# Kernel tuning notes

Hardware: AMD Instinct MI355X
Metric: run time of the kernel (lower is better)

## Reference

```python
import jax, jax.numpy as jnp
import numpy as np

D, H1, O, E = 1024, 4096, 1024, 8
B = 8192


def setup_inputs() -> dict:
    key = jax.random.key(0)
    k1, k2, k3, k4 = jax.random.split(key, 4)
    # kaiming_uniform_ with nonlinearity='relu': bound = sqrt(6 / fan_in), fan_in = last dim
    b_w1 = float(np.sqrt(6.0 / D))
    b_w2 = float(np.sqrt(6.0 / H1))
    x = jax.random.normal(k1, (B, D), dtype=jnp.float32)
    eid = jax.random.randint(k2, (B,), 0, E, dtype=jnp.int32)
    W1 = jax.random.uniform(k3, (E, H1, D), dtype=jnp.float32, minval=-b_w1, maxval=b_w1)
    W2 = jax.random.uniform(k4, (E, O, H1), dtype=jnp.float32, minval=-b_w2, maxval=b_w2)
    b2 = jnp.zeros((E, O), dtype=jnp.float32)
    return {"x": x, "eid": eid, "W1": W1, "W2": W2, "b2": b2}


def reference(x, eid, W1, W2, b2):
    # Per-token expert MLP: y_i = gelu(x_i @ W1[eid_i].T) @ W2[eid_i].T + b2[eid_i]
    # Dense-dispatch formulation: loop over the (small, static) expert axis,
    # compute each expert MLP on all tokens, and select per-token via mask.
    # Math is identical to the sort/gather/scatter original.
    y = jnp.zeros((x.shape[0], W2.shape[1]), dtype=x.dtype)
    for e in range(W1.shape[0]):
        h = jax.nn.gelu(x @ W1[e].T, approximate=False)   # [B, H1]
        y_e = h @ W2[e].T + b2[e]                          # [B, O]
        mask = (eid == e)[:, None].astype(x.dtype)
        y = y + mask * y_e
    return y
```

## Files before the change

kernel.cpp:

```cpp
#include <hip/hip_runtime.h>
#include <hip/hip_bf16.h>
#include <math.h>

constexpr int kD  = 1024;
constexpr int kH1 = 4096;
constexpr int kO  = 1024;
constexpr int kE  = 8;
constexpr int kB  = 8192;

constexpr int BM   = 128;
constexpr int MAXT = kB / BM + kE;

typedef __attribute__((ext_vector_type(8))) short short8;
typedef __attribute__((ext_vector_type(4))) float f32x4;

__device__ __forceinline__ unsigned short f2bf(float f) {
  unsigned int u = __float_as_uint(f);
  u += 0x7fffu + ((u >> 16) & 1u);
  return (unsigned short)(u >> 16);
}

__device__ __forceinline__ float gelu_fast(float x) {
  float u = 0.7978845608028654f * (x + 0.044715f * x * x * x);
  float eu = __expf(2.0f * u);
  float th = 1.0f - 2.0f / (eu + 1.0f);
  return 0.5f * x * (1.0f + th);
}

__device__ __forceinline__ void cvt8(const float* __restrict__ src,
                                     unsigned short* __restrict__ dst) {
  const float4* s = (const float4*)src;
  float4 f0 = s[0], f1 = s[1];
  short8 v;
  v[0] = (short)f2bf(f0.x); v[1] = (short)f2bf(f0.y);
  v[2] = (short)f2bf(f0.z); v[3] = (short)f2bf(f0.w);
  v[4] = (short)f2bf(f1.x); v[5] = (short)f2bf(f1.y);
  v[6] = (short)f2bf(f1.z); v[7] = (short)f2bf(f1.w);
  *(short8*)dst = v;
}

__global__ __launch_bounds__(256) void setup_kernel(const int* __restrict__ eid,
                                                    int* __restrict__ perm,
                                                    int* __restrict__ tiles) {
  __shared__ int cnt[kE];
  __shared__ int off[kE];
  __shared__ int cur[kE];
  int t = threadIdx.x;
  if (t < kE) { cnt[t] = 0; cur[t] = 0; }
  __syncthreads();
  for (int i = t; i < kB; i += 256) atomicAdd(&cnt[eid[i]], 1);
  __syncthreads();
  if (t == 0) {
    int o = 0, nt = 0;
    for (int e = 0; e < kE; ++e) {
      off[e] = o;
      int c = cnt[e];
      for (int r = 0; r < c; r += BM) {
        tiles[nt * 4 + 0] = e;
        tiles[nt * 4 + 1] = o + r;
        tiles[nt * 4 + 2] = (c - r < BM) ? (c - r) : BM;
        tiles[nt * 4 + 3] = 0;
        ++nt;
      }
      o += c;
    }
    for (; nt < MAXT; ++nt) {
      tiles[nt * 4 + 0] = 0; tiles[nt * 4 + 1] = 0;
      tiles[nt * 4 + 2] = 0; tiles[nt * 4 + 3] = 0;
    }
  }
  __syncthreads();
  for (int i = t; i < kB; i += 256) {
    int e = eid[i];
    int p = off[e] + atomicAdd(&cur[e], 1);
    perm[p] = i;
  }
}

constexpr int kGB = kB * kD / 8 / 256;
constexpr int kCN = kE * kH1 * kD / 8;

__global__ __launch_bounds__(256) void prep_kernel(
    const float* __restrict__ x, const int* __restrict__ perm,
    unsigned short* __restrict__ xg,
    const float* __restrict__ W1, unsigned short* __restrict__ W1b) {
  const int b = blockIdx.x;
  if (b < kGB) {
    int idx = b * 256 + threadIdx.x;
    int pos = idx >> 7;
    int c   = (idx & 127) << 3;
    cvt8(x + (size_t)perm[pos] * kD + c, xg + (size_t)pos * kD + c);
  } else {
    const int cb = b - kGB;
    const int stride = 2048 * 256;
    for (int i = cb * 256 + threadIdx.x; i < kCN; i += stride)
      cvt8(W1 + (size_t)i * 8, W1b + (size_t)i * 8);
  }
}

__global__ __launch_bounds__(256) void convert_kernel(const float* __restrict__ src,
                                                      unsigned short* __restrict__ dst,
                                                      int n8) {
  int stride = gridDim.x * 256;
  for (int i = blockIdx.x * 256 + threadIdx.x; i < n8; i += stride)
    cvt8(src + (size_t)i * 8, dst + (size_t)i * 8);
}

template <int KTOT, int N, int NPAN, int MODE, int CONVW2>
__global__ __launch_bounds__(512, 2) void gemm32_kernel(
    const unsigned short* __restrict__ Amat,
    const unsigned short* __restrict__ Bmat,
    const float* __restrict__ bias,
    const int* __restrict__ tiles,
    const int* __restrict__ perm,
    unsigned short* __restrict__ out_bf,
    float* __restrict__ out_f,
    const float* __restrict__ csrc,
    unsigned short* __restrict__ cdst) {
  extern __shared__ char lds[];
  constexpr int NKt = KTOT / 32;
  constexpr int TOTAL = MAXT * NPAN;
  constexpr int cpx = TOTAL / 8;
  constexpr int nchN = (NPAN >= 4) ? NPAN / 4 : 1;

  const int bid = blockIdx.x;
  const int t = threadIdx.x;

  if constexpr (CONVW2 > 0) {
    if (bid >= TOTAL) {
      const int cb = bid - TOTAL;
      constexpr int per = kCN / 512;
      size_t u0 = (size_t)cb * per;
      for (int i = t; i < per; i += 512)
        cvt8(csrc + (u0 + i) * 8, cdst + (u0 + i) * 8);
      return;
    }
  }

  const int id = (bid & 7) * cpx + (bid >> 3);
  const int chunk = id >> 4, a16 = id & 15;
  const int ti = (chunk / nchN) * 4 + (a16 & 3);
  const int n0 = ((chunk % nchN) * 4 + (a16 >> 2)) * 256;

  const int e  = tiles[ti * 4 + 0];
  const int rs = tiles[ti * 4 + 1];
  const int nr = tiles[ti * 4 + 2];
  if (nr == 0) return;

  const int l = t & 63;
  const int w = t >> 6;
  const int lr = l & 15, g = l >> 4;
  const int wr = w >> 2;
  const int wc = w & 3;

  const unsigned short* Bp = Bmat + (size_t)e * N * KTOT;

  const int sR = t >> 2;
  const int sG = (t & 3) ^ ((sR >> 1) & 3);
  const unsigned short* ArowS = Amat + (size_t)(rs + sR) * KTOT + sG * 8;
  const unsigned short* BrowS0 = Bp + (size_t)(n0 + sR) * KTOT + sG * 8;
  const unsigned short* BrowS1 = Bp + (size_t)(n0 + 128 + sR) * KTOT + sG * 8;

  auto stageA = [&](char* buf, int k0) {
    __builtin_amdgcn_global_load_lds(
        (const __attribute__((address_space(1))) unsigned int*)(ArowS + k0),
        (__attribute__((address_space(3))) unsigned int*)(buf + t * 16), 16, 0, 0);
  };
  auto stageB = [&](char* buf, int k0, int i) {
    const unsigned short* src = (i ? BrowS1 : BrowS0) + k0;
    __builtin_amdgcn_global_load_lds(
        (const __attribute__((address_space(1))) unsigned int*)src,
        (__attribute__((address_space(3))) unsigned int*)(buf + 8192 + i * 8192 + t * 16),
        16, 0, 0);
  };

  const int rA = wr * 64 + lr;
  const int rB = wc * 64 + lr;
  const int offA0 = rA * 64 + ((g ^ ((rA >> 1) & 3)) * 16);
  const int offB0 = 8192 + rB * 64 + ((g ^ ((rB >> 1) & 3)) * 16);

  short8 aF[4], bF[4];
  f32x4 acc[4][4] = {};

  char* b0 = lds;
  char* b1 = lds + 24576;
  char* b2 = lds + 49152;

  stageA(b0, 0);  stageB(b0, 0, 0);  stageB(b0, 0, 1);
  stageA(b1, 32); stageB(b1, 32, 0); stageB(b1, 32, 1);

#pragma unroll 1
  for (int kt = 0; kt < NKt; ++kt) {
    const int k0n = (kt + 2) * 32;
    const bool more = (kt + 2 < NKt);
    if (kt == NKt - 1) asm volatile("s_waitcnt vmcnt(0)" ::: "memory");
    else               asm volatile("s_waitcnt vmcnt(3)" ::: "memory");
    __builtin_amdgcn_s_barrier();
    if (more) { stageA(b2, k0n); stageB(b2, k0n, 0); stageB(b2, k0n, 1); }
#pragma unroll
    for (int mr = 0; mr < 4; ++mr)
      aF[mr] = *(const short8*)(b0 + offA0 + mr * 1024);
#pragma unroll
    for (int nc = 0; nc < 4; ++nc)
      bF[nc] = *(const short8*)(b0 + offB0 + nc * 1024);
    __builtin_amdgcn_s_setprio(1);
#pragma unroll
    for (int nc = 0; nc < 4; ++nc)
#pragma unroll
      for (int mr = 0; mr < 4; ++mr)
        acc[nc][mr] = __builtin_amdgcn_mfma_f32_16x16x32_bf16(
            aF[mr], bF[nc], acc[nc][mr], 0, 0, 0);
    __builtin_amdgcn_s_setprio(0);
    char* tmp = b0; b0 = b1; b1 = b2; b2 = tmp;
  }

  const int lr4 = g * 4;
#pragma unroll
  for (int mr = 0; mr < 4; ++mr)
#pragma unroll
    for (int rg = 0; rg < 4; ++rg) {
      int row = wr * 64 + mr * 16 + lr4 + rg;
      if (row < nr) {
        if constexpr (MODE == 0) {
          unsigned short* dst = out_bf + (size_t)(rs + row) * N + n0 + wc * 64;
#pragma unroll
          for (int nc = 0; nc < 4; ++nc)
            dst[nc * 16 + lr] = f2bf(gelu_fast(acc[nc][mr][rg]));
        } else {
          int orig = perm[rs + row];
          float* dst = out_f + (size_t)orig * N + n0 + wc * 64;
          const float* bp = bias + (size_t)e * N + n0 + wc * 64;
#pragma unroll
          for (int nc = 0; nc < 4; ++nc)
            dst[nc * 16 + lr] = acc[nc][mr][rg] + bp[nc * 16 + lr];
        }
      }
    }
}

extern "C" void kernel_launch(void* const* d_in, const int* in_sizes, int n_in,
                              void* d_out, int out_size, void* d_ws, size_t ws_size,
                              hipStream_t stream) {
  const float* x  = (const float*)d_in[0];
  const int*  eid = (const int*)d_in[1];
  const float* W1 = (const float*)d_in[2];
  const float* W2 = (const float*)d_in[3];
  const float* b2 = (const float*)d_in[4];
  float* y = (float*)d_out;

  char* ws = (char*)d_ws;
  int* perm  = (int*)ws;
  int* tiles = (int*)(ws + 32768);
  unsigned short* xg = (unsigned short*)(ws + 36864);
  size_t xg_bytes = (size_t)(kB + 128) * kD * 2;
  unsigned short* h  = (unsigned short*)(ws + 36864 + xg_bytes);
  size_t h_bytes = (size_t)(kB + 128) * kH1 * 2;
  size_t w1b_off = 36864 + xg_bytes + h_bytes;
  unsigned short* W1b = (unsigned short*)(ws + w1b_off);
  size_t w2b_off = w1b_off + 67108864;
  const bool twobuf = ws_size >= w2b_off + 67108864;
  unsigned short* W2b = twobuf ? (unsigned short*)(ws + w2b_off) : W1b;

  auto g1f = gemm32_kernel<kD, kH1, 16, 0, 1>;
  auto g1s = gemm32_kernel<kD, kH1, 16, 0, 0>;
  auto g2  = gemm32_kernel<kH1, kO, 4, 1, 0>;
  (void)hipFuncSetAttribute((const void*)g1f, hipFuncAttributeMaxDynamicSharedMemorySize, 73728);
  (void)hipFuncSetAttribute((const void*)g1s, hipFuncAttributeMaxDynamicSharedMemorySize, 73728);
  (void)hipFuncSetAttribute((const void*)g2,  hipFuncAttributeMaxDynamicSharedMemorySize, 73728);

  setup_kernel<<<1, 256, 0, stream>>>(eid, perm, tiles);

  prep_kernel<<<kGB + 2048, 256, 0, stream>>>(x, perm, xg, W1, W1b);

  if (twobuf) {
    g1f<<<MAXT * 16 + 512, 512, 73728, stream>>>(
        xg, W1b, nullptr, tiles, perm, h, nullptr, W2, W2b);
  } else {
    g1s<<<MAXT * 16, 512, 73728, stream>>>(
        xg, W1b, nullptr, tiles, perm, h, nullptr, nullptr, nullptr);
    convert_kernel<<<2048, 256, 0, stream>>>(W2, W2b, kCN);
  }

  g2<<<MAXT * 4, 512, 73728, stream>>>(
      h, W2b, b2, tiles, perm, nullptr, y, nullptr, nullptr);
}
```

Measured before the change: 312.6 us.

## Switch GEMM inner loop to 32x32x16 MFMA with split-phase staging

Replaces the 16x16x32 bf16 MFMA tiling with 32x32x16 MFMA instructions. Each wave computes its 64x64 tile as 2x2 32x32 blocks, and the LDS fragment offsets and epilogue row mapping are recomputed to match the new accumulator layout. The k-step is split into two phases, each with its own B-fragment loads, interleaved async global->LDS staging, and extra barriers, to spread memory traffic across the MFMA work. The larger MFMA shape should reduce LDS fragment reads per FLOP, but the added barriers and the changed epilogue store pattern may cost throughput.

After: 311.1 us. Within noise of the previous version (-0.5%).

```diff
diff --git a/kernel.cpp b/kernel.cpp
--- a/kernel.cpp
+++ b/kernel.cpp
@@ -12,7 +12,7 @@
 constexpr int MAXT = kB / BM + kE;
 
 typedef __attribute__((ext_vector_type(8))) short short8;
-typedef __attribute__((ext_vector_type(4))) float f32x4;
+typedef __attribute__((ext_vector_type(16))) float f32x16;
 
 __device__ __forceinline__ unsigned short f2bf(float f) {
   unsigned int u = __float_as_uint(f);
@@ -149,7 +149,6 @@
 
   const int l = t & 63;
   const int w = t >> 6;
-  const int lr = l & 15, g = l >> 4;
   const int wr = w >> 2;
   const int wc = w & 3;
 
@@ -174,13 +173,20 @@
         16, 0, 0);
   };
 
-  const int rA = wr * 64 + lr;
-  const int rB = wc * 64 + lr;
-  const int offA0 = rA * 64 + ((g ^ ((rA >> 1) & 3)) * 16);
-  const int offB0 = 8192 + rB * 64 + ((g ^ ((rB >> 1) & 3)) * 16);
-
-  short8 aF[4], bF[4];
-  f32x4 acc[4][4] = {};
+  int offA2[2][2], offB2[2][2];
+#pragma unroll
+  for (int fr = 0; fr < 2; ++fr)
+#pragma unroll
+    for (int ks = 0; ks < 2; ++ks) {
+      int slot = ks * 2 + (l >> 5);
+      int ra = wr * 64 + fr * 32 + (l & 31);
+      offA2[fr][ks] = ra * 64 + ((slot ^ ((ra >> 1) & 3)) * 16);
+      int rb = wc * 64 + fr * 32 + (l & 31);
+      offB2[fr][ks] = 8192 + rb * 64 + ((slot ^ ((rb >> 1) & 3)) * 16);
+    }
+
+  short8 aF[2][2], bF[2];
+  f32x16 acc[2][2] = {};
 
   char* b0 = lds;
   char* b1 = lds + 24576;
@@ -196,43 +202,59 @@
     if (kt == NKt - 1) asm volatile("s_waitcnt vmcnt(0)" ::: "memory");
     else               asm volatile("s_waitcnt vmcnt(3)" ::: "memory");
     __builtin_amdgcn_s_barrier();
-    if (more) { stageA(b2, k0n); stageB(b2, k0n, 0); stageB(b2, k0n, 1); }
-#pragma unroll
-    for (int mr = 0; mr < 4; ++mr)
-      aF[mr] = *(const short8*)(b0 + offA0 + mr * 1024);
-#pragma unroll
-    for (int nc = 0; nc < 4; ++nc)
-      bF[nc] = *(const short8*)(b0 + offB0 + nc * 1024);
+#pragma unroll
+    for (int fr = 0; fr < 2; ++fr)
+#pragma unroll
+      for (int ks = 0; ks < 2; ++ks)
+        aF[fr][ks] = *(const short8*)(b0 + offA2[fr][ks]);
+#pragma unroll
+    for (int ks = 0; ks < 2; ++ks)
+      bF[ks] = *(const short8*)(b0 + offB2[0][ks]);
+    if (more) stageA(b2, k0n);
+    __builtin_amdgcn_s_barrier();
     __builtin_amdgcn_s_setprio(1);
 #pragma unroll
-    for (int nc = 0; nc < 4; ++nc)
-#pragma unroll
-      for (int mr = 0; mr < 4; ++mr)
-        acc[nc][mr] = __builtin_amdgcn_mfma_f32_16x16x32_bf16(
-            aF[mr], bF[nc], acc[nc][mr], 0, 0, 0);
+    for (int fr = 0; fr < 2; ++fr)
+#pragma unroll
+      for (int ks = 0; ks < 2; ++ks)
+        acc[fr][0] = __builtin_amdgcn_mfma_f32_32x32x16_bf16(
+            aF[fr][ks], bF[ks], acc[fr][0], 0, 0, 0);
+    __builtin_amdgcn_s_setprio(0);
+    __builtin_amdgcn_s_barrier();
+#pragma unroll
+    for (int ks = 0; ks < 2; ++ks)
+      bF[ks] = *(const short8*)(b0 + offB2[1][ks]);
+    if (more) { stageB(b2, k0n, 0); stageB(b2, k0n, 1); }
+    __builtin_amdgcn_s_barrier();
+    __builtin_amdgcn_s_setprio(1);
+#pragma unroll
+    for (int fr = 0; fr < 2; ++fr)
+#pragma unroll
+      for (int ks = 0; ks < 2; ++ks)
+        acc[fr][1] = __builtin_amdgcn_mfma_f32_32x32x16_bf16(
+            aF[fr][ks], bF[ks], acc[fr][1], 0, 0, 0);
     __builtin_amdgcn_s_setprio(0);
     char* tmp = b0; b0 = b1; b1 = b2; b2 = tmp;
   }
 
-  const int lr4 = g * 4;
-#pragma unroll
-  for (int mr = 0; mr < 4; ++mr)
-#pragma unroll
-    for (int rg = 0; rg < 4; ++rg) {
-      int row = wr * 64 + mr * 16 + lr4 + rg;
+  const int lc = l & 31;
+  const int r4 = 4 * (l >> 5);
+#pragma unroll
+  for (int fr = 0; fr < 2; ++fr)
+#pragma unroll
+    for (int reg = 0; reg < 16; ++reg) {
+      int row = wr * 64 + fr * 32 + (reg & 3) + 8 * (reg >> 2) + r4;
       if (row < nr) {
         if constexpr (MODE == 0) {
-          unsigned short* dst = out_bf + (size_t)(rs + row) * N + n0 + wc * 64;
-#pragma unroll
-          for (int nc = 0; nc < 4; ++nc)
-            dst[nc * 16 + lr] = f2bf(gelu_fast(acc[nc][mr][rg]));
+          unsigned short* dst = out_bf + (size_t)(rs + row) * N + n0 + wc * 64 + lc;
+          dst[0]  = f2bf(gelu_fast(acc[fr][0][reg]));
+          dst[32] = f2bf(gelu_fast(acc[fr][1][reg]));
         } else {
           int orig = perm[rs + row];
-          float* dst = out_f + (size_t)orig * N + n0 + wc * 64;
-          const float* bp = bias + (size_t)e * N + n0 + wc * 64;
-#pragma unroll
-          for (int nc = 0; nc < 4; ++nc)
-            dst[nc * 16 + lr] = acc[nc][mr][rg] + bp[nc * 16 + lr];
+          float* dst = out_f + (size_t)orig * N + n0 + wc * 64 + lc;
+          const float* bp = bias + (size_t)e * N + n0 + wc * 64 + lc;
+          dst[0]  = acc[fr][0][reg] + bp[0];
+          dst[32] = acc[fr][1][reg] + bp[32];
         }
       }
     }
```
